# Optimization experiments

Hardware: AMD Instinct MI355X
Metric: run time of the kernel (lower is better)

The kernel has to match this reference:

```python
import jax, jax.numpy as jnp
import numpy as np

B, H, M, N, D = 8, 8, 512, 512, 64
HID = 16
MIX1 = (1.0 / 2.0) ** 0.5
MIX2 = (1.0 / 16.0) ** 0.5


def setup_inputs() -> dict:
    key = jax.random.key(0)
    ks = jax.random.split(key, 8)
    q = jax.random.normal(ks[0], (B, H, M, D), dtype=jnp.float32)
    k = jax.random.normal(ks[1], (B, H, N, D), dtype=jnp.float32)
    v = jax.random.normal(ks[2], (B, H, N, D), dtype=jnp.float32)
    dmat = jax.random.uniform(ks[3], (B, M, N), dtype=jnp.float32)
    mix_W1 = jax.random.uniform(ks[4], (H, 2, HID), minval=-MIX1, maxval=MIX1, dtype=jnp.float32)
    mix_b1 = jax.random.uniform(ks[5], (H, HID), minval=-MIX1, maxval=MIX1, dtype=jnp.float32)
    mix_W2 = jax.random.uniform(ks[6], (H, HID, 1), minval=-MIX2, maxval=MIX2, dtype=jnp.float32)
    mix_b2 = jax.random.uniform(ks[7], (H, 1), minval=-MIX2, maxval=MIX2, dtype=jnp.float32)
    return {"q": q, "k": k, "v": v, "dmat": dmat,
            "mix_W1": mix_W1, "mix_b1": mix_b1, "mix_W2": mix_W2, "mix_b2": mix_b2}


def reference(q, k, v, dmat, mix_W1, mix_b1, mix_W2, mix_b2):
    # attention scores: [b,h,m,n]
    scale = 1.0 / jnp.sqrt(jnp.float32(k.shape[-1]))
    scores = jnp.einsum("bhmd,bhnd->bhmn", q, k) * scale
    # stack dot-product scores with distance matrix: [b,h,m,n,2]
    mixed = jnp.stack([scores, jnp.broadcast_to(dmat[:, None, :, :], scores.shape)], axis=-1)
    # per-head 2-layer MLP over the 2-channel axis
    h1 = jax.nn.relu(jnp.einsum("bhmnc,hcf->bhmnf", mixed, mix_W1)
                     + mix_b1[None, :, None, None, :])          # [b,h,m,n,HID]
    mixed_scores = (jnp.einsum("bhmnf,hfo->bhmno", h1, mix_W2)[..., 0]
                    + mix_b2[None, :, None, None, 0])            # [b,h,m,n]
    attn = jax.nn.softmax(mixed_scores, axis=-1)
    return jnp.einsum("bhmn,bhnd->bhmd", attn, v)
```

## Files before the change

kernel.cpp:

```cpp
#include <hip/hip_runtime.h>
#include <hip/hip_bf16.h>


typedef __attribute__((ext_vector_type(4))) float f32x4;
typedef __attribute__((ext_vector_type(8))) __bf16 bf16x8;
typedef __attribute__((ext_vector_type(4))) __bf16 bf16x4;

static __device__ __forceinline__ float rlf(float x) {
    return __uint_as_float(__builtin_amdgcn_readfirstlane(__float_as_uint(x)));
}
static __device__ __forceinline__ void cvt2(float x, __bf16& h, __bf16& l) {
    h = (__bf16)x;
    l = (__bf16)(x - (float)h);
}
static __device__ __forceinline__ int sw64(int row, int col) {
    return row * 64 + ((((col >> 3) ^ (row & 7)) << 3) | (col & 7));
}
static __device__ __forceinline__ void dma16(const __bf16* g, __bf16* l) {
    __builtin_amdgcn_global_load_lds(
        (const __attribute__((address_space(1))) unsigned*)g,
        (__attribute__((address_space(3))) unsigned*)l, 16, 0, 0);
}

#define B_ 8
#define H_ 8
#define M_ 512
#define N_ 512
#define D_ 64
#define HID_ 16

__global__ __launch_bounds__(256) void prep_kernel(
    const float* __restrict__ kg, const float* __restrict__ vg,
    __bf16* __restrict__ ws)
{
    __shared__ float vld[64 * 68];
    const int t   = threadIdx.x;
    const int blk = blockIdx.x;
    const long base = (long)blk * 4096;
    __bf16* out = ws + (long)blk * 16384;

#pragma unroll
    for (int it = 0; it < 4; ++it) {
        const int e = it * 1024 + t * 4;
        const int rr = e >> 6, c0 = e & 63;
        f32x4 v4 = *(const f32x4*)(vg + base + e);
        *(f32x4*)(vld + rr * 68 + c0) = v4;
    }

#pragma unroll
    for (int qq = t; qq < 512; qq += 256) {
        const int row = qq >> 3, c = qq & 7;
        const float* src = kg + base + row * 64 + ((c ^ (row & 7)) << 3);
        f32x4 a = *(const f32x4*)src;
        f32x4 b4 = *(const f32x4*)(src + 4);
        bf16x8 hv, lv;
#pragma unroll
        for (int j = 0; j < 4; ++j) {
            __bf16 h, l;
            cvt2(a[j], h, l);  hv[j] = h;     lv[j] = l;
            cvt2(b4[j], h, l); hv[4 + j] = h; lv[4 + j] = l;
        }
        *(bf16x8*)(out + qq * 8) = hv;
        *(bf16x8*)(out + 4096 + qq * 8) = lv;
    }
    __syncthreads();

#pragma unroll
    for (int qq = t; qq < 512; qq += 256) {
        const int d = qq & 63, c = qq >> 6;
        bf16x8 hv, lv;
#pragma unroll
        for (int dd = 0; dd < 2; ++dd) {
            const int nb = (((2 * c + dd) ^ (d & 15)) << 2);
#pragma unroll
            for (int jj = 0; jj < 4; ++jj) {
                __bf16 h, l;
                cvt2(vld[(nb + jj) * 68 + d], h, l);
                hv[dd * 4 + jj] = h; lv[dd * 4 + jj] = l;
            }
        }
        const int pos = d * 64 + c * 8;
        *(bf16x8*)(out + 8192 + pos) = hv;
        *(bf16x8*)(out + 12288 + pos) = lv;
    }
}

__global__ __launch_bounds__(512, 4) void msdpa_kernel(
    const float* __restrict__ qg, const __bf16* __restrict__ ws,
    const float* __restrict__ dg, const float* __restrict__ w1g,
    const float* __restrict__ b1g, const float* __restrict__ w2g,
    float* __restrict__ outg)
{
    extern __shared__ __bf16 smem[];
    float* xm  = (float*)(smem + 32768);
    float* xls = xm + 128;

    const int tid  = threadIdx.x;
    const int lane = tid & 63;
    const int wv   = tid >> 6;
    const int r16  = lane & 15;
    const int g    = lane >> 4;
    const int rw   = wv & 3;
    const int hn   = wv >> 2;

    const int bm = blockIdx.x;
    const int h  = blockIdx.y;
    const int b  = blockIdx.z;

    const long bh = (long)(b * H_ + h);
    const __bf16* wsbh = ws + bh * (8L * 16384);

    __bf16* bcur = smem;
    __bf16* bnxt = smem + 16384;

#pragma unroll
    for (int i = 0; i < 4; ++i)
        dma16(wsbh + i * 4096 + tid * 8, bcur + i * 4096 + tid * 8);

    const float* w1h = w1g + h * 2 * HID_;
    const float* b1h = b1g + h * HID_;
    const float* w2h = w2g + h * HID_;
    float af[HID_], cf[HID_], bf_[HID_], wa[HID_];
    float A = 0.f, C = 0.f, B0 = 0.f;
#pragma unroll
    for (int f = 0; f < HID_; ++f) {
        af[f] = rlf(w1h[f]) * 0.125f;
        cf[f] = rlf(w1h[HID_ + f]);
        bf_[f] = rlf(b1h[f]);
        wa[f] = rlf(w2h[f]) * (1.4426950408889634f * 0.5f);
        A  = fmaf(wa[f], af[f], A);
        C  = fmaf(wa[f], cf[f], C);
        B0 = fmaf(wa[f], bf_[f], B0);
    }

    const float* qbase = qg + (bh * M_ + (long)bm * 64 + rw * 16 + r16) * D_;
    bf16x8 qh[2], ql[2];
#pragma unroll
    for (int ks = 0; ks < 2; ++ks) {
        f32x4 x0 = *(const f32x4*)(qbase + ks * 32 + g * 8);
        f32x4 x1 = *(const f32x4*)(qbase + ks * 32 + g * 8 + 4);
        bf16x8 hv, lv;
#pragma unroll
        for (int j = 0; j < 4; ++j) {
            __bf16 h_, l_;
            cvt2(x0[j], h_, l_); hv[j] = h_; lv[j] = l_;
            cvt2(x1[j], h_, l_); hv[4 + j] = h_; lv[4 + j] = l_;
        }
        qh[ks] = hv; ql[ks] = lv;
    }

    const float* dmp = dg + ((long)b * M_ + (long)bm * 64 + rw * 16 + r16) * N_
                          + hn * 32 + g * 4;
    f32x4 dmvc[2], dmvn[2];
#pragma unroll
    for (int n16 = 0; n16 < 2; ++n16)
        dmvc[n16] = *(const f32x4*)(dmp + n16 * 16);

    f32x4 oacc[4];
#pragma unroll
    for (int dt = 0; dt < 4; ++dt) oacc[dt] = f32x4{0.f, 0.f, 0.f, 0.f};
    float mrun = -1e30f, lsum = 0.0f;

    __syncthreads();

    for (int nt = 0; nt < 8; ++nt) {
        if (nt < 7) {
            const __bf16* tile = wsbh + (nt + 1) * 16384;
#pragma unroll
            for (int i = 0; i < 4; ++i)
                dma16(tile + i * 4096 + tid * 8, bnxt + i * 4096 + tid * 8);
#pragma unroll
            for (int n16 = 0; n16 < 2; ++n16)
                dmvn[n16] = *(const f32x4*)(dmp + (nt + 1) * 64 + n16 * 16);
        }

        __bf16* KH  = bcur;
        __bf16* KL  = bcur + 4096;
        __bf16* VTH = bcur + 8192;
        __bf16* VTL = bcur + 12288;

        f32x4 sacc[2];
#pragma unroll
        for (int n16 = 0; n16 < 2; ++n16) sacc[n16] = f32x4{0.f, 0.f, 0.f, 0.f};
#pragma unroll
        for (int n16 = 0; n16 < 2; ++n16) {
            const int row = hn * 32 + n16 * 16 + r16;
#pragma unroll
            for (int ks = 0; ks < 2; ++ks) {
                const int off = sw64(row, ks * 32 + g * 8);
                bf16x8 kh_ = *(const bf16x8*)(KH + off);
                bf16x8 kl_ = *(const bf16x8*)(KL + off);
                sacc[n16] = __builtin_amdgcn_mfma_f32_16x16x32_bf16(kh_, qh[ks], sacc[n16], 0, 0, 0);
                sacc[n16] = __builtin_amdgcn_mfma_f32_16x16x32_bf16(kh_, ql[ks], sacc[n16], 0, 0, 0);
                sacc[n16] = __builtin_amdgcn_mfma_f32_16x16x32_bf16(kl_, qh[ks], sacc[n16], 0, 0, 0);
            }
        }

        float ms[2][4];
#pragma unroll
        for (int n16 = 0; n16 < 2; ++n16)
#pragma unroll
            for (int r = 0; r < 4; ++r) {
                const float s = sacc[n16][r], d = dmvc[n16][r];
                float acc = fmaf(A, s, fmaf(C, d, B0));
#pragma unroll
                for (int f = 0; f < HID_; ++f) {
                    const float u = fmaf(af[f], s, fmaf(cf[f], d, bf_[f]));
                    acc = fmaf(wa[f], fabsf(u), acc);
                }
                ms[n16][r] = acc;
            }

        float mloc = fmaxf(fmaxf(fmaxf(ms[0][0], ms[0][1]), fmaxf(ms[0][2], ms[0][3])),
                           fmaxf(fmaxf(ms[1][0], ms[1][1]), fmaxf(ms[1][2], ms[1][3])));
        mloc = fmaxf(mloc, __shfl_xor(mloc, 16));
        mloc = fmaxf(mloc, __shfl_xor(mloc, 32));
        float p[8], psum = 0.f;
#pragma unroll
        for (int n16 = 0; n16 < 2; ++n16)
#pragma unroll
            for (int r = 0; r < 4; ++r) {
                const float pv = exp2f(ms[n16][r] - mloc);
                p[n16 * 4 + r] = pv;
                psum += pv;
            }
        if (g == 0) xm[wv * 16 + r16] = mloc;
        __syncthreads();

        const float mloc2 = xm[(wv ^ 4) * 16 + r16];
        const float mnew = fmaxf(mrun, fmaxf(mloc, mloc2));
        const float scO  = exp2f(mrun - mnew);
        const float fac1 = exp2f(mloc - mnew);
        mrun = mnew;
        lsum = fmaf(lsum, scO, psum * fac1);

        bf16x8 pa, pb;
#pragma unroll
        for (int j = 0; j < 8; ++j) {
            __bf16 h_, l_;
            cvt2(p[j] * fac1, h_, l_);
            pa[j] = h_; pb[j] = l_;
        }

        float scm[4];
#pragma unroll
        for (int r = 0; r < 4; ++r) scm[r] = __shfl(scO, g * 4 + r);
#pragma unroll
        for (int dt = 0; dt < 4; ++dt)
#pragma unroll
            for (int r = 0; r < 4; ++r) oacc[dt][r] *= scm[r];

#pragma unroll
        for (int dt = 0; dt < 4; ++dt) {
            const int rowb = (dt * 16 + r16) * 64;
            const int p0 = ((hn * 8 + g) ^ r16) * 4;
            const int p1 = ((hn * 8 + 4 + g) ^ r16) * 4;
            bf16x4 vh0 = *(const bf16x4*)(VTH + rowb + p0);
            bf16x4 vh1 = *(const bf16x4*)(VTH + rowb + p1);
            bf16x4 vl0 = *(const bf16x4*)(VTL + rowb + p0);
            bf16x4 vl1 = *(const bf16x4*)(VTL + rowb + p1);
            bf16x8 vh = __builtin_shufflevector(vh0, vh1, 0, 1, 2, 3, 4, 5, 6, 7);
            bf16x8 vl = __builtin_shufflevector(vl0, vl1, 0, 1, 2, 3, 4, 5, 6, 7);
            oacc[dt] = __builtin_amdgcn_mfma_f32_16x16x32_bf16(pa, vh, oacc[dt], 0, 0, 0);
            oacc[dt] = __builtin_amdgcn_mfma_f32_16x16x32_bf16(pa, vl, oacc[dt], 0, 0, 0);
            oacc[dt] = __builtin_amdgcn_mfma_f32_16x16x32_bf16(pb, vh, oacc[dt], 0, 0, 0);
        }

        __syncthreads();
        __bf16* tmp = bcur; bcur = bnxt; bnxt = tmp;
#pragma unroll
        for (int n16 = 0; n16 < 2; ++n16) dmvc[n16] = dmvn[n16];
    }

    lsum += __shfl_xor(lsum, 16);
    lsum += __shfl_xor(lsum, 32);

    float* obuf = (float*)smem;
    if (hn == 1) {
        if (g == 0) xls[rw * 16 + r16] = lsum;
#pragma unroll
        for (int dt = 0; dt < 4; ++dt)
#pragma unroll
            for (int r = 0; r < 4; ++r)
                obuf[rw * 1024 + (g * 4 + r) * 64 + dt * 16 + r16] = oacc[dt][r];
    }
    __syncthreads();
    if (hn == 0) {
        const float Ltot = lsum + xls[rw * 16 + r16];
        float linv[4];
#pragma unroll
        for (int r = 0; r < 4; ++r) linv[r] = 1.0f / __shfl(Ltot, g * 4 + r);
        float* obase = outg + (bh * M_ + (long)bm * 64 + rw * 16) * D_;
#pragma unroll
        for (int dt = 0; dt < 4; ++dt)
#pragma unroll
            for (int r = 0; r < 4; ++r) {
                const float o2 = obuf[rw * 1024 + (g * 4 + r) * 64 + dt * 16 + r16];
                obase[(g * 4 + r) * D_ + dt * 16 + r16] = (oacc[dt][r] + o2) * linv[r];
            }
    }
}

extern "C" void kernel_launch(void* const* d_in, const int* in_sizes, int n_in,
                              void* d_out, int out_size, void* d_ws, size_t ws_size,
                              hipStream_t stream) {
    const float* q  = (const float*)d_in[0];
    const float* k  = (const float*)d_in[1];
    const float* v  = (const float*)d_in[2];
    const float* dm = (const float*)d_in[3];
    const float* w1 = (const float*)d_in[4];
    const float* b1 = (const float*)d_in[5];
    const float* w2 = (const float*)d_in[6];
    float* out = (float*)d_out;
    __bf16* ws = (__bf16*)d_ws;

    prep_kernel<<<dim3(512), dim3(256), 0, stream>>>(k, v, ws);

    (void)hipFuncSetAttribute(reinterpret_cast<const void*>(msdpa_kernel),
                              hipFuncAttributeMaxDynamicSharedMemorySize, 66560);
    dim3 grid(M_ / 64, H_, B_);
    msdpa_kernel<<<grid, dim3(512), 66560, stream>>>(q, ws, dm, w1, b1, w2, out);
}
```

Measured before the change: 137.9 us.

## Compute mixing MLP in packed fp16 and keep independent per-half softmax maxima

```diff
diff --git a/kernel.cpp b/kernel.cpp
--- a/kernel.cpp
+++ b/kernel.cpp
@@ -5,6 +5,9 @@
 typedef __attribute__((ext_vector_type(4))) float f32x4;
 typedef __attribute__((ext_vector_type(8))) __bf16 bf16x8;
 typedef __attribute__((ext_vector_type(4))) __bf16 bf16x4;
+typedef __attribute__((ext_vector_type(2))) _Float16 h16x2;
+
+union HU { h16x2 h; unsigned u; };
 
 static __device__ __forceinline__ float rlf(float x) {
     return __uint_as_float(__builtin_amdgcn_readfirstlane(__float_as_uint(x)));
@@ -92,8 +95,7 @@
     float* __restrict__ outg)
 {
     extern __shared__ __bf16 smem[];
-    float* xm  = (float*)(smem + 32768);
-    float* xls = xm + 128;
+    float* xm = (float*)(smem + 32768);
 
     const int tid  = threadIdx.x;
     const int lane = tid & 63;
@@ -132,6 +134,14 @@
         C  = fmaf(wa[f], cf[f], C);
         B0 = fmaf(wa[f], bf_[f], B0);
     }
+    h16x2 af2[8], cf2[8], bf2[8], wa2[8];
+#pragma unroll
+    for (int fp = 0; fp < 8; ++fp) {
+        af2[fp] = h16x2{(_Float16)af[2 * fp], (_Float16)af[2 * fp + 1]};
+        cf2[fp] = h16x2{(_Float16)cf[2 * fp], (_Float16)cf[2 * fp + 1]};
+        bf2[fp] = h16x2{(_Float16)bf_[2 * fp], (_Float16)bf_[2 * fp + 1]};
+        wa2[fp] = h16x2{(_Float16)wa[2 * fp], (_Float16)wa[2 * fp + 1]};
+    }
 
     const float* qbase = qg + (bh * M_ + (long)bm * 64 + rw * 16 + r16) * D_;
     bf16x8 qh[2], ql[2];
@@ -202,11 +212,15 @@
 #pragma unroll
             for (int r = 0; r < 4; ++r) {
                 const float s = sacc[n16][r], d = dmvc[n16][r];
+                const _Float16 sh = (_Float16)s, dh = (_Float16)d;
+                const h16x2 s2 = h16x2{sh, sh}, d2 = h16x2{dh, dh};
                 float acc = fmaf(A, s, fmaf(C, d, B0));
 #pragma unroll
-                for (int f = 0; f < HID_; ++f) {
-                    const float u = fmaf(af[f], s, fmaf(cf[f], d, bf_[f]));
-                    acc = fmaf(wa[f], fabsf(u), acc);
+                for (int fp = 0; fp < 8; ++fp) {
+                    h16x2 u2 = __builtin_elementwise_fma(
+                        af2[fp], s2, __builtin_elementwise_fma(cf2[fp], d2, bf2[fp]));
+                    HU hu; hu.h = u2; hu.u &= 0x7FFF7FFFu;
+                    acc = __builtin_amdgcn_fdot2(wa2[fp], hu.h, acc, false);
                 }
                 ms[n16][r] = acc;
             }
@@ -215,6 +229,11 @@
                            fmaxf(fmaxf(ms[1][0], ms[1][1]), fmaxf(ms[1][2], ms[1][3])));
         mloc = fmaxf(mloc, __shfl_xor(mloc, 16));
         mloc = fmaxf(mloc, __shfl_xor(mloc, 32));
+        const float mnew = fmaxf(mrun, mloc);
+        const float scO  = exp2f(mrun - mnew);
+        const float fac1 = exp2f(mloc - mnew);
+        mrun = mnew;
+
         float p[8], psum = 0.f;
 #pragma unroll
         for (int n16 = 0; n16 < 2; ++n16)
@@ -224,14 +243,6 @@
                 p[n16 * 4 + r] = pv;
                 psum += pv;
             }
-        if (g == 0) xm[wv * 16 + r16] = mloc;
-        __syncthreads();
-
-        const float mloc2 = xm[(wv ^ 4) * 16 + r16];
-        const float mnew = fmaxf(mrun, fmaxf(mloc, mloc2));
-        const float scO  = exp2f(mrun - mnew);
-        const float fac1 = exp2f(mloc - mnew);
-        mrun = mnew;
         lsum = fmaf(lsum, scO, psum * fac1);
 
         bf16x8 pa, pb;
@@ -277,7 +288,7 @@
 
     float* obuf = (float*)smem;
     if (hn == 1) {
-        if (g == 0) xls[rw * 16 + r16] = lsum;
+        if (g == 0) { xm[rw * 16 + r16] = mrun; xm[64 + rw * 16 + r16] = lsum; }
 #pragma unroll
         for (int dt = 0; dt < 4; ++dt)
 #pragma unroll
@@ -286,17 +297,27 @@
     }
     __syncthreads();
     if (hn == 0) {
-        const float Ltot = lsum + xls[rw * 16 + r16];
-        float linv[4];
-#pragma unroll
-        for (int r = 0; r < 4; ++r) linv[r] = 1.0f / __shfl(Ltot, g * 4 + r);
+        const float m2 = xm[rw * 16 + r16];
+        const float l2 = xm[64 + rw * 16 + r16];
+        const float mstar = fmaxf(mrun, m2);
+        const float a1 = exp2f(mrun - mstar);
+        const float a2 = exp2f(m2 - mstar);
+        const float linv = 1.0f / fmaf(lsum, a1, l2 * a2);
+        const float w1r_ = a1 * linv, w2r_ = a2 * linv;
+        float w1r[4], w2r[4];
+#pragma unroll
+        for (int r = 0; r < 4; ++r) {
+            w1r[r] = __shfl(w1r_, g * 4 + r);
+            w2r[r] = __shfl(w2r_, g * 4 + r);
+        }
         float* obase = outg + (bh * M_ + (long)bm * 64 + rw * 16) * D_;
 #pragma unroll
         for (int dt = 0; dt < 4; ++dt)
 #pragma unroll
             for (int r = 0; r < 4; ++r) {
                 const float o2 = obuf[rw * 1024 + (g * 4 + r) * 64 + dt * 16 + r16];
-                obase[(g * 4 + r) * D_ + dt * 16 + r16] = (oacc[dt][r] + o2) * linv[r];
+                obase[(g * 4 + r) * D_ + dt * 16 + r16] =
+                    fmaf(oacc[dt][r], w1r[r], o2 * w2r[r]);
             }
     }
 }
```

After: 134.2 us. -2.6%, faster.
